# Kernel tuning notes

Hardware: AMD Instinct MI355X
Metric: run time of the kernel (lower is better)

The kernel has to match this reference:

```python
import jax, jax.numpy as jnp
import numpy as np

B, T, D = 4, 4096, 1024
P = 64  # d_model / n_head

def setup_inputs() -> dict:
    key = jax.random.key(0)
    k1, k2, k3 = jax.random.split(key, 3)
    x = jax.random.normal(k1, (B, T, D), dtype=jnp.float32)
    Wqkv = jax.random.normal(k2, (D, 3 * P), dtype=jnp.float32) * (1.0 / np.sqrt(D))
    bqkv = jax.random.normal(k3, (3 * P,), dtype=jnp.float32) * 0.01
    return {"x": x, "Wqkv": Wqkv, "bqkv": bqkv}

def reference(x, Wqkv, bqkv):
    Bv, Tv, Cv = x.shape
    qkv = (x @ Wqkv + bqkv).reshape(Bv, Tv, 3, P)  # [B,T,3,p]
    q, k, v = qkv[:, :, 0, :], qkv[:, :, 1, :], qkv[:, :, 2, :]
    # raw scores (source applies NO 1/sqrt(p) scaling)
    S = jnp.einsum('btp,bsp->bts', q, k)  # [B,T,T]
    causal = jnp.tril(jnp.ones((Tv, Tv), dtype=bool))
    S = jnp.where(causal[None, :, :], S, jnp.float32(-jnp.inf))
    Pm = jax.nn.softmax(S, axis=-1)
    O = jnp.einsum('bts,bsp->btp', Pm, v)  # [B,T,p]
    return O
```

## Files before the change

### kernel.cpp

```cpp
#include <hip/hip_runtime.h>
#include <hip/hip_fp16.h>

#define B_ 4
#define T_ 4096
#define D_ 1024

typedef _Float16 h8 __attribute__((ext_vector_type(8)));
typedef _Float16 h4 __attribute__((ext_vector_type(4)));
typedef float f32x4 __attribute__((ext_vector_type(4)));

#define LOG2E 1.44269504088896340736f
#define MASKV -3.0e38f
#define MINIT -1.0e30f
#define EXP2(x) __builtin_amdgcn_exp2f(x)

__global__ __launch_bounds__(256) void wt_kernel(const float* __restrict__ W,
                                                 _Float16* __restrict__ Wt) {
    __shared__ _Float16 Tr[192][20];
    const int tid = threadIdx.x, k0 = blockIdx.x * 16;
#pragma unroll
    for (int i = 0; i < 3; i++) {
        int fi = tid + 256 * i;
        int r = fi / 48, c4 = fi % 48;
        float4 v = *(const float4*)(W + (size_t)(k0 + r) * 192 + c4 * 4);
        Tr[c4 * 4 + 0][r] = (_Float16)v.x;
        Tr[c4 * 4 + 1][r] = (_Float16)v.y;
        Tr[c4 * 4 + 2][r] = (_Float16)v.z;
        Tr[c4 * 4 + 3][r] = (_Float16)v.w;
    }
    __syncthreads();
#pragma unroll
    for (int i = 0; i < 3; i++) {
        int oi = tid + 256 * i;
        int n = oi >> 2, kq = oi & 3;
        *(h4*)(Wt + (size_t)n * D_ + k0 + kq * 4) = *(const h4*)&Tr[n][kq * 4];
    }
}

__global__ __launch_bounds__(256) void proj_kernel(
    const float* __restrict__ x, const _Float16* __restrict__ Wt,
    const float* __restrict__ bias,
    _Float16* __restrict__ qh, _Float16* __restrict__ kh, _Float16* __restrict__ vh)
{
    __shared__ _Float16 As[2][32][72];
    __shared__ _Float16 Bs[2][96][72];
    const int tid = threadIdx.x;
    const int w = tid >> 6, lane = tid & 63, quad = lane >> 4, l16 = lane & 15;
    const int row0 = (blockIdx.x >> 1) * 32;
    const int nb0 = (blockIdx.x & 1) * 96;
    const int mstrip = w & 1;
    const int ngrp = (w >> 1) * 3;

    float bvals[3];
#pragma unroll
    for (int nt = 0; nt < 3; nt++) bvals[nt] = bias[nb0 + (ngrp + nt) * 16 + l16];

    f32x4 acc[3];
#pragma unroll
    for (int i = 0; i < 3; i++) acc[i] = (f32x4){0.f, 0.f, 0.f, 0.f};

    const int arow = tid >> 3, ac0 = (tid & 7) * 8;

    float4 xa, xb;
    h8 wreg[3];
    {
        const float* xp = x + (size_t)(row0 + arow) * D_ + ac0;
        xa = *(const float4*)xp; xb = *(const float4*)(xp + 4);
#pragma unroll
        for (int p = 0; p < 3; p++) {
            int f = tid + 256 * p; int n = f >> 3, c0 = (f & 7) * 8;
            wreg[p] = *(const h8*)(Wt + (size_t)(nb0 + n) * D_ + c0);
        }
    }

    for (int kc = 0; kc < 16; kc++) {
        const int buf = kc & 1;
        h8 av;
        av[0]=(_Float16)xa.x; av[1]=(_Float16)xa.y; av[2]=(_Float16)xa.z; av[3]=(_Float16)xa.w;
        av[4]=(_Float16)xb.x; av[5]=(_Float16)xb.y; av[6]=(_Float16)xb.z; av[7]=(_Float16)xb.w;
        *(h8*)&As[buf][arow][ac0] = av;
#pragma unroll
        for (int p = 0; p < 3; p++) {
            int f = tid + 256 * p; int n = f >> 3, c0 = (f & 7) * 8;
            *(h8*)&Bs[buf][n][c0] = wreg[p];
        }
        if (kc + 1 < 16) {
            int k0 = (kc + 1) * 64;
            const float* xp = x + (size_t)(row0 + arow) * D_ + k0 + ac0;
            xa = *(const float4*)xp; xb = *(const float4*)(xp + 4);
#pragma unroll
            for (int p = 0; p < 3; p++) {
                int f = tid + 256 * p; int n = f >> 3, c0 = (f & 7) * 8;
                wreg[p] = *(const h8*)(Wt + (size_t)(nb0 + n) * D_ + k0 + c0);
            }
        }
        __syncthreads();
        h8 a0 = *(const h8*)&As[buf][16 * mstrip + l16][quad * 8];
        h8 a1 = *(const h8*)&As[buf][16 * mstrip + l16][32 + quad * 8];
#pragma unroll
        for (int nt = 0; nt < 3; nt++) {
            h8 b0 = *(const h8*)&Bs[buf][(ngrp + nt) * 16 + l16][quad * 8];
            h8 b1 = *(const h8*)&Bs[buf][(ngrp + nt) * 16 + l16][32 + quad * 8];
            acc[nt] = __builtin_amdgcn_mfma_f32_16x16x32_f16(a0, b0, acc[nt], 0, 0, 0);
            acc[nt] = __builtin_amdgcn_mfma_f32_16x16x32_f16(a1, b1, acc[nt], 0, 0, 0);
        }
    }

#pragma unroll
    for (int nt = 0; nt < 3; nt++) {
        int n = nb0 + (ngrp + nt) * 16 + l16;
        int g = n >> 6, p = n & 63;
        _Float16* dst = (g == 0) ? qh : (g == 1) ? kh : vh;
        float scale = (g == 0) ? LOG2E : 1.0f;
#pragma unroll
        for (int reg = 0; reg < 4; reg++) {
            int trow = row0 + 16 * mstrip + quad * 4 + reg;
            dst[(size_t)trow * 64 + p] = (_Float16)((acc[nt][reg] + bvals[nt]) * scale);
        }
    }
}

__global__ __launch_bounds__(256, 4) void attn_kernel(
    const _Float16* __restrict__ qh, const _Float16* __restrict__ kh,
    const _Float16* __restrict__ vh, float* __restrict__ out,
    _Float16* __restrict__ Opart, float2* __restrict__ ml,
    int lgC, int NC1, int direct)
{
    __shared__ _Float16 Ks[2][64][72];
    __shared__ _Float16 Vt[2][64][72];
    const int tid = threadIdx.x;
    const int w = tid >> 6, lane = tid & 63, quad = lane >> 4, l16 = lane & 15;
    const int C = 1 << lgC;

    const int cid = blockIdx.x;
    const int b = cid / NC1;
    int rem = cid - b * NC1;
    int qt2 = 0, k0 = 0, cnt = 1;
    for (int i = 0; i < 32; i++) {
        int nc = (2 * i + 2 + C - 1) >> lgC;
        if (rem < nc) { qt2 = i; k0 = rem << lgC; cnt = min(C, 2 * i + 2 - k0); break; }
        rem -= nc;
    }
    const size_t base = (size_t)b * T_ * 64;
    const int qbase = qt2 * 128 + w * 32;

    h8 qf[2][2];
#pragma unroll
    for (int u = 0; u < 2; u++) {
        const _Float16* qp = qh + base + (size_t)(qbase + u * 16 + l16) * 64 + quad * 8;
        qf[u][0] = *(const h8*)qp;
        qf[u][1] = *(const h8*)(qp + 32);
    }

    f32x4 o[8];
#pragma unroll
    for (int i = 0; i < 8; i++) o[i] = (f32x4){0.f, 0.f, 0.f, 0.f};
    float m[2] = {MINIT, MINIT}, l[2] = {0.f, 0.f};

    const int krow = tid >> 3, kc0 = (tid & 7) * 8;
    const int vp0 = (tid & 15) * 4, vc0 = (tid >> 4) * 4;
    h8 kreg[2];
    h4 vreg[4];
    {
        const _Float16* kp = kh + base + (size_t)(k0 * 64) * 64;
        kreg[0] = *(const h8*)(kp + (size_t)krow * 64 + kc0);
        kreg[1] = *(const h8*)(kp + (size_t)(krow + 32) * 64 + kc0);
        const _Float16* vp = vh + base + (size_t)(k0 * 64 + vc0) * 64 + vp0;
#pragma unroll
        for (int i = 0; i < 4; i++) vreg[i] = *(const h4*)(vp + (size_t)i * 64);
    }

    const int kend = k0 + cnt;
    for (int kt = k0; kt < kend; kt++) {
        const int buf = kt & 1;
        *(h8*)&Ks[buf][krow][kc0] = kreg[0];
        *(h8*)&Ks[buf][krow + 32][kc0] = kreg[1];
#pragma unroll
        for (int j = 0; j < 4; j++) {
            h4 t;
            t[0] = vreg[0][j]; t[1] = vreg[1][j]; t[2] = vreg[2][j]; t[3] = vreg[3][j];
            *(h4*)&Vt[buf][vp0 + j][vc0] = t;
        }
        if (kt + 1 < kend) {
            const _Float16* kp = kh + base + (size_t)((kt + 1) * 64) * 64;
            kreg[0] = *(const h8*)(kp + (size_t)krow * 64 + kc0);
            kreg[1] = *(const h8*)(kp + (size_t)(krow + 32) * 64 + kc0);
            const _Float16* vp = vh + base + (size_t)((kt + 1) * 64 + vc0) * 64 + vp0;
#pragma unroll
            for (int i = 0; i < 4; i++) vreg[i] = *(const h4*)(vp + (size_t)i * 64);
        }
        __syncthreads();

        const bool skip = (kt * 64) > (qbase + 31);
        if (!skip) {
            f32x4 s[2][4];
#pragma unroll
            for (int nt = 0; nt < 4; nt++) {
                h8 kf0 = *(const h8*)&Ks[buf][nt * 16 + l16][quad * 8];
                h8 kf1 = *(const h8*)&Ks[buf][nt * 16 + l16][32 + quad * 8];
#pragma unroll
                for (int u = 0; u < 2; u++) {
                    f32x4 c = (f32x4){0.f, 0.f, 0.f, 0.f};
                    c = __builtin_amdgcn_mfma_f32_16x16x32_f16(kf0, qf[u][0], c, 0, 0, 0);
                    c = __builtin_amdgcn_mfma_f32_16x16x32_f16(kf1, qf[u][1], c, 0, 0, 0);
                    s[u][nt] = c;
                }
            }

            h4 pf[2][4];
#pragma unroll
            for (int u = 0; u < 2; u++) {
                const int qrow = qbase + u * 16 + l16;
                if (kt * 64 + 63 > qbase + u * 16) {
#pragma unroll
                    for (int nt = 0; nt < 4; nt++)
#pragma unroll
                        for (int reg = 0; reg < 4; reg++) {
                            int sg = kt * 64 + nt * 16 + quad * 4 + reg;
                            if (sg > qrow) s[u][nt][reg] = MASKV;
                        }
                }
                float mx = s[u][0][0];
#pragma unroll
                for (int nt = 0; nt < 4; nt++)
#pragma unroll
                    for (int reg = 0; reg < 4; reg++) mx = fmaxf(mx, s[u][nt][reg]);
                mx = fmaxf(mx, __shfl_xor(mx, 16));
                mx = fmaxf(mx, __shfl_xor(mx, 32));
                float mnew = fmaxf(m[u], mx);
                float alpha = EXP2(m[u] - mnew);
                m[u] = mnew;
                float rs = 0.f;
#pragma unroll
                for (int nt = 0; nt < 4; nt++) {
#pragma unroll
                    for (int reg = 0; reg < 4; reg++) {
                        float p = EXP2(s[u][nt][reg] - mnew);
                        s[u][nt][reg] = p;
                        rs += p;
                    }
                    h4 ph;
                    ph[0]=(_Float16)s[u][nt][0]; ph[1]=(_Float16)s[u][nt][1];
                    ph[2]=(_Float16)s[u][nt][2]; ph[3]=(_Float16)s[u][nt][3];
                    pf[u][nt] = ph;
                }
                rs += __shfl_xor(rs, 16);
                rs += __shfl_xor(rs, 32);
                l[u] = l[u] * alpha + rs;
#pragma unroll
                for (int pt = 0; pt < 4; pt++)
#pragma unroll
                    for (int reg = 0; reg < 4; reg++) o[u * 4 + pt][reg] *= alpha;
            }

#pragma unroll
            for (int pt = 0; pt < 4; pt++)
#pragma unroll
                for (int nt = 0; nt < 4; nt++) {
                    h4 vf = *(const h4*)&Vt[buf][pt * 16 + l16][nt * 16 + quad * 4];
                    o[pt]     = __builtin_amdgcn_mfma_f32_16x16x16f16(vf, pf[0][nt], o[pt], 0, 0, 0);
                    o[4 + pt] = __builtin_amdgcn_mfma_f32_16x16x16f16(vf, pf[1][nt], o[4 + pt], 0, 0, 0);
                }
        }
    }

    if (direct) {
#pragma unroll
        for (int u = 0; u < 2; u++) {
            float linv = 1.0f / l[u];
            int trow = qt2 * 128 + w * 32 + u * 16 + l16;
#pragma unroll
            for (int pt = 0; pt < 4; pt++)
#pragma unroll
                for (int reg = 0; reg < 4; reg++)
                    out[base + (size_t)trow * 64 + pt * 16 + quad * 4 + reg] =
                        o[u * 4 + pt][reg] * linv;
        }
    } else {
        _Float16* op = Opart + (size_t)cid * 8192;
#pragma unroll
        for (int u = 0; u < 2; u++) {
            int r = w * 32 + u * 16 + l16;
#pragma unroll
            for (int pt = 0; pt < 4; pt++) {
                h4 ph;
#pragma unroll
                for (int reg = 0; reg < 4; reg++) ph[reg] = (_Float16)o[u * 4 + pt][reg];
                *(h4*)(op + (size_t)r * 64 + pt * 16 + quad * 4) = ph;
            }
            if (quad == 0) ml[(size_t)cid * 128 + r] = make_float2(m[u], l[u]);
        }
    }
}

__global__ __launch_bounds__(256) void combine_kernel(
    const _Float16* __restrict__ Opart, const float2* __restrict__ ml,
    float* __restrict__ out, int lgC, int NC1)
{
    const int C = 1 << lgC;
    const int task = blockIdx.x;
    const int b = task >> 8, tile = (task >> 3) & 31, rg = task & 7;
    int pref = 0;
    for (int i = 0; i < tile; i++) pref += (2 * i + 2 + C - 1) >> lgC;
    const int cbase = b * NC1 + pref;
    const int nch = (2 * tile + 2 + C - 1) >> lgC;

    const int r = rg * 16 + (threadIdx.x >> 4);
    const int c0 = (threadIdx.x & 15) * 4;

    float M = MINIT;
    for (int i = 0; i < nch; i++) M = fmaxf(M, ml[(size_t)(cbase + i) * 128 + r].x);
    float L = 0.f, acc[4] = {0.f, 0.f, 0.f, 0.f};
    for (int i = 0; i < nch; i++) {
        float2 v = ml[(size_t)(cbase + i) * 128 + r];
        float sc = EXP2(v.x - M);
        L += sc * v.y;
        h4 x4 = *(const h4*)(Opart + (size_t)(cbase + i) * 8192 + (size_t)r * 64 + c0);
#pragma unroll
        for (int t = 0; t < 4; t++) acc[t] += sc * (float)x4[t];
    }
    float inv = 1.0f / L;
    float4 res = { acc[0]*inv, acc[1]*inv, acc[2]*inv, acc[3]*inv };
    *(float4*)(out + ((size_t)b * T_ + tile * 128 + r) * 64 + c0) = res;
}

extern "C" void kernel_launch(void* const* d_in, const int* in_sizes, int n_in,
                              void* d_out, int out_size, void* d_ws, size_t ws_size,
                              hipStream_t stream) {
    const float* x    = (const float*)d_in[0];
    const float* W    = (const float*)d_in[1];
    const float* bias = (const float*)d_in[2];
    float* out = (float*)d_out;
    char* ws = (char*)d_ws;
    _Float16* qh = (_Float16*)(ws);
    _Float16* kh = (_Float16*)(ws + (size_t)2 * 1024 * 1024);
    _Float16* vh = (_Float16*)(ws + (size_t)4 * 1024 * 1024);
    _Float16* Wt = (_Float16*)(ws + (size_t)6 * 1024 * 1024);
    const size_t pbase = (size_t)8 * 1024 * 1024;

    int lgC = -1, nc1 = 32;
    for (int lg = 2; lg <= 6; lg++) {
        int C = 1 << lg, n1 = 0;
        for (int i = 0; i < 32; i++) n1 += (2 * i + 2 + C - 1) >> lg;
        size_t need = pbase + (size_t)4 * n1 * (8192 * 2 + 128 * 8);
        if (need <= ws_size) { lgC = lg; nc1 = n1; break; }
    }
    int direct = (lgC < 0) ? 1 : 0;
    if (direct) { lgC = 6; nc1 = 32; }
    _Float16* Opart = (_Float16*)(ws + pbase);
    float2*   mlp   = (float2*)(ws + pbase + (size_t)4 * nc1 * 8192 * 2);

    wt_kernel<<<64, 256, 0, stream>>>(W, Wt);
    proj_kernel<<<1024, 256, 0, stream>>>(x, Wt, bias, qh, kh, vh);
    attn_kernel<<<4 * nc1, 256, 0, stream>>>(qh, kh, vh, out, Opart, mlp, lgC, nc1, direct);
    if (!direct)
        combine_kernel<<<1024, 256, 0, stream>>>(Opart, mlp, out, lgC, nc1);
}
```

Measured before the change: 176.2 us.

## Widen projection tile, stage outputs via LDS, remap attention blocks, raise min chunk

The projection kernel now computes all 192 output columns per block with 32-wide k-steps, so x is read once instead of twice. Results are staged through shared memory so the q/k/v stores become contiguous 16-byte writes. The attention kernel permutes block ids across 8 groups (XCD-style interleave) and stages its partial outputs through LDS for coalesced writes. The minimum split-K chunk rises from 4 to 8, cutting partial traffic and combine work at the cost of less parallelism and more LDS use in the projection.

```diff
diff --git a/kernel.cpp b/kernel.cpp
--- a/kernel.cpp
+++ b/kernel.cpp
@@ -42,81 +42,81 @@
     const float* __restrict__ bias,
     _Float16* __restrict__ qh, _Float16* __restrict__ kh, _Float16* __restrict__ vh)
 {
-    __shared__ _Float16 As[2][32][72];
-    __shared__ _Float16 Bs[2][96][72];
+    __shared__ _Float16 As[2][32][40];
+    __shared__ _Float16 Bs[2][192][40];
+    __shared__ _Float16 Ost[32][200];
     const int tid = threadIdx.x;
     const int w = tid >> 6, lane = tid & 63, quad = lane >> 4, l16 = lane & 15;
-    const int row0 = (blockIdx.x >> 1) * 32;
-    const int nb0 = (blockIdx.x & 1) * 96;
+    const int row0 = blockIdx.x * 32;
     const int mstrip = w & 1;
-    const int ngrp = (w >> 1) * 3;
-
-    float bvals[3];
-#pragma unroll
-    for (int nt = 0; nt < 3; nt++) bvals[nt] = bias[nb0 + (ngrp + nt) * 16 + l16];
-
-    f32x4 acc[3];
-#pragma unroll
-    for (int i = 0; i < 3; i++) acc[i] = (f32x4){0.f, 0.f, 0.f, 0.f};
-
-    const int arow = tid >> 3, ac0 = (tid & 7) * 8;
-
-    float4 xa, xb;
+    const int ngrp = (w >> 1) * 6;
+
+    float bvals[6];
+#pragma unroll
+    for (int nt = 0; nt < 6; nt++) bvals[nt] = bias[(ngrp + nt) * 16 + l16];
+
+    f32x4 acc[6];
+#pragma unroll
+    for (int i = 0; i < 6; i++) acc[i] = (f32x4){0.f, 0.f, 0.f, 0.f};
+
+    const int arow = tid >> 3, ac0 = (tid & 7) * 4;
+
+    float4 xa;
     h8 wreg[3];
     {
-        const float* xp = x + (size_t)(row0 + arow) * D_ + ac0;
-        xa = *(const float4*)xp; xb = *(const float4*)(xp + 4);
+        xa = *(const float4*)(x + (size_t)(row0 + arow) * D_ + ac0);
 #pragma unroll
         for (int p = 0; p < 3; p++) {
-            int f = tid + 256 * p; int n = f >> 3, c0 = (f & 7) * 8;
-            wreg[p] = *(const h8*)(Wt + (size_t)(nb0 + n) * D_ + c0);
-        }
-    }
-
-    for (int kc = 0; kc < 16; kc++) {
+            int f = tid + 256 * p; int n = f >> 2, c0 = (f & 3) * 8;
+            wreg[p] = *(const h8*)(Wt + (size_t)n * D_ + c0);
+        }
+    }
+
+    for (int kc = 0; kc < 32; kc++) {
         const int buf = kc & 1;
-        h8 av;
+        h4 av;
         av[0]=(_Float16)xa.x; av[1]=(_Float16)xa.y; av[2]=(_Float16)xa.z; av[3]=(_Float16)xa.w;
-        av[4]=(_Float16)xb.x; av[5]=(_Float16)xb.y; av[6]=(_Float16)xb.z; av[7]=(_Float16)xb.w;
-        *(h8*)&As[buf][arow][ac0] = av;
+        *(h4*)&As[buf][arow][ac0] = av;
 #pragma unroll
         for (int p = 0; p < 3; p++) {
-            int f = tid + 256 * p; int n = f >> 3, c0 = (f & 7) * 8;
+            int f = tid + 256 * p; int n = f >> 2, c0 = (f & 3) * 8;
             *(h8*)&Bs[buf][n][c0] = wreg[p];
         }
-        if (kc + 1 < 16) {
-            int k0 = (kc + 1) * 64;
-            const float* xp = x + (size_t)(row0 + arow) * D_ + k0 + ac0;
-            xa = *(const float4*)xp; xb = *(const float4*)(xp + 4);
+        if (kc + 1 < 32) {
+            int k0 = (kc + 1) * 32;
+            xa = *(const float4*)(x + (size_t)(row0 + arow) * D_ + k0 + ac0);
 #pragma unroll
             for (int p = 0; p < 3; p++) {
-                int f = tid + 256 * p; int n = f >> 3, c0 = (f & 7) * 8;
-                wreg[p] = *(const h8*)(Wt + (size_t)(nb0 + n) * D_ + k0 + c0);
+                int f = tid + 256 * p; int n = f >> 2, c0 = (f & 3) * 8;
+                wreg[p] = *(const h8*)(Wt + (size_t)n * D_ + k0 + c0);
             }
         }
         __syncthreads();
         h8 a0 = *(const h8*)&As[buf][16 * mstrip + l16][quad * 8];
-        h8 a1 = *(const h8*)&As[buf][16 * mstrip + l16][32 + quad * 8];
-#pragma unroll
-        for (int nt = 0; nt < 3; nt++) {
+#pragma unroll
+        for (int nt = 0; nt < 6; nt++) {
             h8 b0 = *(const h8*)&Bs[buf][(ngrp + nt) * 16 + l16][quad * 8];
-            h8 b1 = *(const h8*)&Bs[buf][(ngrp + nt) * 16 + l16][32 + quad * 8];
             acc[nt] = __builtin_amdgcn_mfma_f32_16x16x32_f16(a0, b0, acc[nt], 0, 0, 0);
-            acc[nt] = __builtin_amdgcn_mfma_f32_16x16x32_f16(a1, b1, acc[nt], 0, 0, 0);
-        }
-    }
-
-#pragma unroll
-    for (int nt = 0; nt < 3; nt++) {
-        int n = nb0 + (ngrp + nt) * 16 + l16;
-        int g = n >> 6, p = n & 63;
-        _Float16* dst = (g == 0) ? qh : (g == 1) ? kh : vh;
-        float scale = (g == 0) ? LOG2E : 1.0f;
-#pragma unroll
-        for (int reg = 0; reg < 4; reg++) {
-            int trow = row0 + 16 * mstrip + quad * 4 + reg;
-            dst[(size_t)trow * 64 + p] = (_Float16)((acc[nt][reg] + bvals[nt]) * scale);
-        }
+        }
+    }
+
+#pragma unroll
+    for (int nt = 0; nt < 6; nt++) {
+        int n = (ngrp + nt) * 16 + l16;
+        float scale = (n < 64) ? LOG2E : 1.0f;
+#pragma unroll
+        for (int reg = 0; reg < 4; reg++)
+            Ost[16 * mstrip + quad * 4 + reg][n] =
+                (_Float16)((acc[nt][reg] + bvals[nt]) * scale);
+    }
+    __syncthreads();
+    {
+        const int mrow = tid >> 3, c0 = (tid & 7) * 8;
+        _Float16* dsts[3] = {qh, kh, vh};
+#pragma unroll
+        for (int g = 0; g < 3; g++)
+            *(h8*)(dsts[g] + (size_t)(row0 + mrow) * 64 + c0) =
+                *(const h8*)&Ost[mrow][g * 64 + c0];
     }
 }
 
@@ -124,7 +124,7 @@
     const _Float16* __restrict__ qh, const _Float16* __restrict__ kh,
     const _Float16* __restrict__ vh, float* __restrict__ out,
     _Float16* __restrict__ Opart, float2* __restrict__ ml,
-    int lgC, int NC1, int direct)
+    int lgC, int NC1, int direct, int q8, int total)
 {
     __shared__ _Float16 Ks[2][64][72];
     __shared__ _Float16 Vt[2][64][72];
@@ -132,7 +132,10 @@
     const int w = tid >> 6, lane = tid & 63, quad = lane >> 4, l16 = lane & 15;
     const int C = 1 << lgC;
 
-    const int cid = blockIdx.x;
+    const int bid = blockIdx.x;
+    const int cid = (bid & 7) * q8 + (bid >> 3);
+    if (cid >= total) return;
+
     const int b = cid / NC1;
     int rem = cid - b * NC1;
     int qt2 = 0, k0 = 0, cnt = 1;
@@ -277,7 +280,8 @@
                         o[u * 4 + pt][reg] * linv;
         }
     } else {
-        _Float16* op = Opart + (size_t)cid * 8192;
+        __syncthreads();
+        _Float16* St = &Ks[0][0][0];
 #pragma unroll
         for (int u = 0; u < 2; u++) {
             int r = w * 32 + u * 16 + l16;
@@ -286,10 +290,16 @@
                 h4 ph;
 #pragma unroll
                 for (int reg = 0; reg < 4; reg++) ph[reg] = (_Float16)o[u * 4 + pt][reg];
-                *(h4*)(op + (size_t)r * 64 + pt * 16 + quad * 4) = ph;
+                *(h4*)&St[r * 72 + pt * 16 + quad * 4] = ph;
             }
             if (quad == 0) ml[(size_t)cid * 128 + r] = make_float2(m[u], l[u]);
         }
+        __syncthreads();
+        _Float16* op = Opart + (size_t)cid * 8192;
+        const int r = tid >> 1, c0 = (tid & 1) * 32;
+#pragma unroll
+        for (int j = 0; j < 4; j++)
+            *(h8*)(op + r * 64 + c0 + 8 * j) = *(const h8*)&St[r * 72 + c0 + 8 * j];
     }
 }
 
@@ -339,7 +349,7 @@
     const size_t pbase = (size_t)8 * 1024 * 1024;
 
     int lgC = -1, nc1 = 32;
-    for (int lg = 2; lg <= 6; lg++) {
+    for (int lg = 3; lg <= 6; lg++) {
         int C = 1 << lg, n1 = 0;
         for (int i = 0; i < 32; i++) n1 += (2 * i + 2 + C - 1) >> lg;
         size_t need = pbase + (size_t)4 * n1 * (8192 * 2 + 128 * 8);
@@ -350,9 +360,13 @@
     _Float16* Opart = (_Float16*)(ws + pbase);
     float2*   mlp   = (float2*)(ws + pbase + (size_t)4 * nc1 * 8192 * 2);
 
+    const int total = 4 * nc1;
+    const int q8 = (total + 7) / 8;
+
     wt_kernel<<<64, 256, 0, stream>>>(W, Wt);
-    proj_kernel<<<1024, 256, 0, stream>>>(x, Wt, bias, qh, kh, vh);
-    attn_kernel<<<4 * nc1, 256, 0, stream>>>(qh, kh, vh, out, Opart, mlp, lgC, nc1, direct);
+    proj_kernel<<<512, 256, 0, stream>>>(x, Wt, bias, qh, kh, vh);
+    attn_kernel<<<8 * q8, 256, 0, stream>>>(qh, kh, vh, out, Opart, mlp,
+                                            lgC, nc1, direct, q8, total);
     if (!direct)
         combine_kernel<<<1024, 256, 0, stream>>>(Opart, mlp, out, lgC, nc1);
 }
```

After: 166.6 us. -5.5%, faster.
